# Optimization experiments

Hardware: AMD Instinct MI355X
Metric: run time of the kernel (lower is better)

The kernel has to match this reference:

```python
import jax, jax.numpy as jnp
import numpy as np

N = 50000   # num_nodes
E = 640000  # num_edges (avg degree ~12.8)
D = 128     # input_dim
H = 128     # hidden_dim
T = 100     # targets per head


def setup_inputs() -> dict:
    key = jax.random.key(0)
    ks = jax.random.split(key, 20)
    w = lambda k, s: jax.random.normal(k, s, jnp.float32) * 0.02
    return {
        "x": jax.random.normal(ks[0], (N, D), jnp.float32),
        "edge_index": jax.random.randint(ks[1], (2, E), 0, N, dtype=jnp.int32),
        "edge_weight": jax.random.uniform(ks[2], (E,), jnp.float32),
        "ace_idx": jax.random.randint(ks[3], (T,), 0, N, dtype=jnp.int32),
        "h2_idx": jax.random.randint(ks[4], (T,), 0, N, dtype=jnp.int32),
        "W1": w(ks[5], (D, H)), "b1": jnp.zeros((H,), jnp.float32),
        "W2": w(ks[6], (H, H)), "b2": jnp.zeros((H,), jnp.float32),
        "W3": w(ks[7], (H, H)), "b3": jnp.zeros((H,), jnp.float32),
        "Wh": w(ks[8], (H, H)), "bh": jnp.zeros((H,), jnp.float32),
        "Wace": w(ks[9], (H, 1)), "bace": jnp.zeros((1,), jnp.float32),
        "Wh2": w(ks[10], (H, 1)), "bh2": jnp.zeros((1,), jnp.float32),
    }


def gcn_conv(x, src, dst, ew, W, b):
    # PyG GCNConv: add self-loops (weight 1), symmetric D^-1/2 (A+I) D^-1/2, then XW + b
    n = x.shape[0]
    xw = x @ W                                             # [N, H]
    deg = jax.ops.segment_sum(ew, dst, num_segments=n) + 1.0  # +1 from self-loop
    dinv = jax.lax.rsqrt(jnp.maximum(deg, 1e-12))          # deg >= 1 here
    norm = dinv[src] * ew * dinv[dst]                      # per-edge coefficient
    agg = jax.ops.segment_sum(norm[:, None] * xw[src], dst, num_segments=n)
    agg = agg + (dinv * dinv)[:, None] * xw                # self-loop contribution
    return agg + b


def reference(x, edge_index, edge_weight, ace_idx, h2_idx,
              W1, b1, W2, b2, W3, b3, Wh, bh, Wace, bace, Wh2, bh2):
    src, dst = edge_index[0], edge_index[1]
    h = jax.nn.relu(gcn_conv(x, src, dst, edge_weight, W1, b1))
    h = jax.nn.relu(gcn_conv(h, src, dst, edge_weight, W2, b2))
    h = jax.nn.relu(gcn_conv(h, src, dst, edge_weight, W3, b3))
    # dropout is identity in eval mode
    h = jax.nn.relu(h @ Wh + bh)
    ace_pred = h[ace_idx] @ Wace + bace   # [T, 1]
    h2_pred = h[h2_idx] @ Wh2 + bh2       # [T, 1]
    return jnp.concatenate([ace_pred, h2_pred], axis=0)  # [2T, 1]
```

## Files before the change

### kernel.cpp

```cpp
#include <hip/hip_runtime.h>
#include <math.h>

constexpr int N = 50000;
constexpr int E = 640000;
constexpr int D = 128;
constexpr int T = 100;
constexpr int MAXDEG = 64;
constexpr float SC = 256.0f;
constexpr float SCINV = 1.0f / 256.0f;
constexpr int GB = (N + 127) / 128;
constexpr int EB = (E + 255) / 256;
constexpr int WB = 2 * 16384 / 256;

typedef __attribute__((ext_vector_type(8))) _Float16 half8v;
typedef __attribute__((ext_vector_type(8))) unsigned short ushort8v;
typedef __attribute__((ext_vector_type(4))) float f32x4;

__device__ inline float dinv_of(unsigned int degY) {
  return 1.0f / sqrtf((float)degY * (1.0f / 16777216.0f) + 1.0f);
}


template <bool DINV>
__device__ inline void mfma_core_and_store(
    const unsigned short* __restrict__ Bl, half8v (*a)[2],
    const uint2* __restrict__ degcnt,
    int row0, int rbase, int q, int n16, unsigned short* __restrict__ out) {
  constexpr int SB = 136;
  f32x4 acc[2][8] = {};
#pragma unroll
  for (int kc = 0; kc < 4; ++kc) {
    const int ko = kc * 32 + q * 8;
#pragma unroll
    for (int ct = 0; ct < 8; ++ct) {
      int n = ct * 16 + n16;
      half8v b = *(const half8v*)&Bl[n * SB + ko];
#pragma unroll
      for (int rt = 0; rt < 2; ++rt) {
        acc[rt][ct] = __builtin_amdgcn_mfma_f32_16x16x32_f16(a[kc][rt], b, acc[rt][ct], 0, 0, 0);
      }
    }
  }
#pragma unroll
  for (int rt = 0; rt < 2; ++rt) {
#pragma unroll
    for (int r = 0; r < 4; ++r) {
      int gr = row0 + rbase + rt * 16 + q * 4 + r;
      if (gr < N) {
        float dv = 1.0f;
        if (DINV) dv = dinv_of(degcnt[gr].y);
#pragma unroll
        for (int ct = 0; ct < 8; ++ct) {
          int col = ct * 16 + n16;
          _Float16 h = (_Float16)(DINV ? acc[rt][ct][r] * dv : acc[rt][ct][r]);
          out[(size_t)gr * D + col] = *(unsigned short*)&h;
        }
      }
    }
  }
}


__global__ __launch_bounds__(256) void fused_build_kernel(
    const float* __restrict__ x, const float* __restrict__ W1,
    const float* __restrict__ W2, const float* __restrict__ W3,
    const float* __restrict__ ew, const int* __restrict__ src,
    const int* __restrict__ dst,
    unsigned long long* __restrict__ degcnt, unsigned int* __restrict__ slot,
    unsigned short* __restrict__ wt1, unsigned short* __restrict__ w3kn,
    unsigned short* __restrict__ z1) {
  constexpr int SB = 136;
  __shared__ unsigned short Bl[128 * SB];
  const int b = blockIdx.x;
  const int tid = threadIdx.x;

  if (b < GB) {
#pragma unroll
    for (int it = 0; it < 16; ++it) {
      int idx4 = tid + it * 256;
      int e = idx4 * 4;
      int k = e >> 7, n = e & 127;
      float4 v = *(const float4*)&W1[e];
      _Float16 h0 = (_Float16)(v.x * SC);
      _Float16 h1 = (_Float16)(v.y * SC);
      _Float16 h2 = (_Float16)(v.z * SC);
      _Float16 h3 = (_Float16)(v.w * SC);
      Bl[(n + 0) * SB + k] = *(unsigned short*)&h0;
      Bl[(n + 1) * SB + k] = *(unsigned short*)&h1;
      Bl[(n + 2) * SB + k] = *(unsigned short*)&h2;
      Bl[(n + 3) * SB + k] = *(unsigned short*)&h3;
    }
    __syncthreads();

    const int w = tid >> 6, lane = tid & 63;
    const int q = lane >> 4, n16 = lane & 15;
    const int rbase = w * 32;
    const int row0 = b * 128;
    size_t arow[2];
#pragma unroll
    for (int rt = 0; rt < 2; ++rt) {
      int gr = row0 + rbase + rt * 16 + n16;
      if (gr >= N) gr = N - 1;
      arow[rt] = (size_t)gr * D;
    }
    half8v a[4][2];
#pragma unroll
    for (int kc = 0; kc < 4; ++kc) {
      const int ko = kc * 32 + q * 8;
#pragma unroll
      for (int rt = 0; rt < 2; ++rt) {
        float4 v0 = *(const float4*)&x[arow[rt] + ko];
        float4 v1 = *(const float4*)&x[arow[rt] + ko + 4];
        half8v h;
        h[0] = (_Float16)v0.x; h[1] = (_Float16)v0.y;
        h[2] = (_Float16)v0.z; h[3] = (_Float16)v0.w;
        h[4] = (_Float16)v1.x; h[5] = (_Float16)v1.y;
        h[6] = (_Float16)v1.z; h[7] = (_Float16)v1.w;
        a[kc][rt] = h;
      }
    }
    mfma_core_and_store<false>(Bl, a, nullptr, row0, rbase, q, n16, z1);
  } else if (b < GB + EB) {
    int e = (b - GB) * 256 + tid;
    if (e < E) {
      float w = ew[e];
      int d = dst[e];
      unsigned int fxdeg = __float2uint_rn(w * 16777216.0f);
      unsigned int fx16 = __float2uint_rn(w * 65536.0f);
      if (fx16 > 65535u) fx16 = 65535u;
      unsigned long long old = atomicAdd(&degcnt[d],
                                         ((unsigned long long)fxdeg << 32) | 1ull);
      unsigned int rank = (unsigned int)(old & 0xffffffffull);
      if (rank < MAXDEG)
        slot[(size_t)d * MAXDEG + rank] = (fx16 << 16) | (unsigned int)src[e];
    }
  } else {
    int idx = (b - GB - EB) * 256 + tid;
    int layer = idx >> 14;
    int r = idx & 16383;
    int k = r & 127, n = r >> 7;
    if (layer == 0) {
      _Float16 h = (_Float16)W2[k * D + n];
      wt1[n * D + k] = *(unsigned short*)&h;
    } else {
      _Float16 h = (_Float16)W3[k * D + n];
      w3kn[k * D + n] = *(unsigned short*)&h;
    }
  }
}


__device__ inline void stage_B(const unsigned short* __restrict__ Wt,
                               unsigned short* __restrict__ Bl, int tid) {
  constexpr int SB = 136;
#pragma unroll
  for (int it = 0; it < 8; ++it) {
    int idx = tid + it * 256;
    int r = idx >> 4;
    int c8 = idx & 15;
    ushort8v v = *(const ushort8v*)&Wt[r * D + c8 * 8];
    *(ushort8v*)&Bl[r * SB + c8 * 8] = v;
  }
}

__global__ __launch_bounds__(256) void gemm_mfma_kernel(
    const unsigned short* __restrict__ A, const unsigned short* __restrict__ Wt,
    const uint2* __restrict__ degcnt, unsigned short* __restrict__ out) {
  constexpr int SB = 136;
  __shared__ unsigned short Bl[128 * SB];
  const int tid = threadIdx.x;
  const int row0 = blockIdx.x * 128;
  stage_B(Wt, Bl, tid);
  __syncthreads();

  const int w = tid >> 6, lane = tid & 63;
  const int q = lane >> 4, n16 = lane & 15;
  const int rbase = w * 32;
  size_t arow[2];
#pragma unroll
  for (int rt = 0; rt < 2; ++rt) {
    int gr = row0 + rbase + rt * 16 + n16;
    if (gr >= N) gr = N - 1;
    arow[rt] = (size_t)gr * D;
  }
  half8v a[4][2];
#pragma unroll
  for (int kc = 0; kc < 4; ++kc) {
    const int ko = kc * 32 + q * 8;
#pragma unroll
    for (int rt = 0; rt < 2; ++rt)
      a[kc][rt] = *(const half8v*)&A[arow[rt] + ko];
  }
  mfma_core_and_store<true>(Bl, a, degcnt, row0, rbase, q, n16, out);
}


__global__ __launch_bounds__(256) void agg_kernel(
    const unsigned short* __restrict__ z, const unsigned int* __restrict__ slot,
    const uint2* __restrict__ degcnt, const float* __restrict__ bias,
    unsigned short* __restrict__ oP) {
  int g = (blockIdx.x * 256 + threadIdx.x) >> 4;
  int lane = threadIdx.x & 15;
  const unsigned int* degY = (const unsigned int*)degcnt;

  uint2 pg = degcnt[g];
  int cnt = (int)pg.x; if (cnt > MAXDEG) cnt = MAXDEG;
  float dvg = dinv_of(pg.y);
  half8v xv = *(const half8v*)&z[(size_t)g * D + lane * 8];
  float acc[8];
#pragma unroll
  for (int i = 0; i < 8; ++i) acc[i] = dvg * (float)xv[i];

  const unsigned int* sl = slot + (size_t)g * MAXDEG;
  int k = 0;
  for (; k + 4 <= cnt; k += 4) {
    uint4 p = *(const uint4*)&sl[k];
    float d0 = dinv_of(degY[((p.x & 0xffffu) << 1) + 1]);
    float d1 = dinv_of(degY[((p.y & 0xffffu) << 1) + 1]);
    float d2 = dinv_of(degY[((p.z & 0xffffu) << 1) + 1]);
    float d3 = dinv_of(degY[((p.w & 0xffffu) << 1) + 1]);
    float c0 = (float)(p.x >> 16) * (1.0f / 65536.0f) * d0;
    float c1 = (float)(p.y >> 16) * (1.0f / 65536.0f) * d1;
    float c2 = (float)(p.z >> 16) * (1.0f / 65536.0f) * d2;
    float c3 = (float)(p.w >> 16) * (1.0f / 65536.0f) * d3;
    half8v v0 = *(const half8v*)&z[(size_t)(p.x & 0xffffu) * D + lane * 8];
    half8v v1 = *(const half8v*)&z[(size_t)(p.y & 0xffffu) * D + lane * 8];
    half8v v2 = *(const half8v*)&z[(size_t)(p.z & 0xffffu) * D + lane * 8];
    half8v v3 = *(const half8v*)&z[(size_t)(p.w & 0xffffu) * D + lane * 8];
#pragma unroll
    for (int i = 0; i < 8; ++i) {
      acc[i] = fmaf(c0, (float)v0[i], acc[i]);
      acc[i] = fmaf(c1, (float)v1[i], acc[i]);
      acc[i] = fmaf(c2, (float)v2[i], acc[i]);
      acc[i] = fmaf(c3, (float)v3[i], acc[i]);
    }
  }
  for (; k < cnt; ++k) {
    unsigned int p = sl[k];
    float dsv = dinv_of(degY[((p & 0xffffu) << 1) + 1]);
    float c = (float)(p >> 16) * (1.0f / 65536.0f) * dsv;
    half8v v = *(const half8v*)&z[(size_t)(p & 0xffffu) * D + lane * 8];
#pragma unroll
    for (int i = 0; i < 8; ++i) acc[i] = fmaf(c, (float)v[i], acc[i]);
  }

  half8v hv;
#pragma unroll
  for (int i = 0; i < 8; ++i)
    hv[i] = (_Float16)fmaxf(fmaf(dvg, acc[i], bias[lane * 8 + i] * SC), 0.f);
  *(half8v*)&oP[(size_t)g * D + lane * 8] = hv;
}


__global__ __launch_bounds__(256) void l23_heads_kernel(
    const unsigned short* __restrict__ z2, const unsigned int* __restrict__ slot,
    const uint2* __restrict__ degcnt,
    const float* __restrict__ b2, const float* __restrict__ b3,
    const unsigned short* __restrict__ w3kn,
    const float* __restrict__ Wh, const float* __restrict__ bh,
    const int* __restrict__ ace_idx, const int* __restrict__ h2_idx,
    const float* __restrict__ Wace, const float* __restrict__ bace,
    const float* __restrict__ Wh2, const float* __restrict__ bh2,
    float* __restrict__ out) {
  __shared__ float sacc[16][128];
  __shared__ unsigned short w3l[16384];
  __shared__ float svec[128];
  __shared__ float h3v[128];
  __shared__ float psum[2];
  int t = blockIdx.x;
  int tid = threadIdx.x;
  int node; const float* whead; float bhead;
  if (t < T) { node = ace_idx[t];     whead = Wace; bhead = bace[0]; }
  else       { node = h2_idx[t - T];  whead = Wh2;  bhead = bh2[0]; }

#pragma unroll
  for (int it = 0; it < 8; ++it) {
    int idx = tid + it * 256;
    *(ushort8v*)&w3l[idx * 8] = *(const ushort8v*)&w3kn[idx * 8];
  }

  int grp = tid >> 4, lane = tid & 15;
  float b2l[8];
#pragma unroll
  for (int i = 0; i < 8; ++i) b2l[i] = b2[lane * 8 + i] * SC;

  uint2 pn = degcnt[node];
  int tcnt = (int)pn.x; if (tcnt > MAXDEG) tcnt = MAXDEG;
  float dvn = dinv_of(pn.y);
  const unsigned int* tsl = slot + (size_t)node * MAXDEG;
  int nitems = 1 + tcnt;
  float a[8] = {};
  for (int it = grp; it < nitems; it += 16) {
    int u; float wgt;
    if (it == 0) { u = node; wgt = 1.0f; }
    else {
      unsigned int p = tsl[it - 1];
      wgt = (float)(p >> 16) * (1.0f / 65536.0f);
      u = (int)(p & 0xffffu);
    }
    uint2 pu = degcnt[u];
    float dvu = dinv_of(pu.y);
    int cu = (int)pu.x; if (cu > MAXDEG) cu = MAXDEG;
    half8v xv = *(const half8v*)&z2[(size_t)u * D + lane * 8];
    float r[8];
#pragma unroll
    for (int i = 0; i < 8; ++i) r[i] = (float)xv[i];
    const unsigned int* usl = slot + (size_t)u * MAXDEG;
    int e = 0;
    for (; e + 4 <= cu; e += 4) {
      uint4 p4 = *(const uint4*)&usl[e];
      float c0 = (float)(p4.x >> 16) * (1.0f / 65536.0f);
      float c1 = (float)(p4.y >> 16) * (1.0f / 65536.0f);
      float c2 = (float)(p4.z >> 16) * (1.0f / 65536.0f);
      float c3 = (float)(p4.w >> 16) * (1.0f / 65536.0f);
      half8v v0 = *(const half8v*)&z2[(size_t)(p4.x & 0xffffu) * D + lane * 8];
      half8v v1 = *(const half8v*)&z2[(size_t)(p4.y & 0xffffu) * D + lane * 8];
      half8v v2 = *(const half8v*)&z2[(size_t)(p4.z & 0xffffu) * D + lane * 8];
      half8v v3 = *(const half8v*)&z2[(size_t)(p4.w & 0xffffu) * D + lane * 8];
#pragma unroll
      for (int i = 0; i < 8; ++i) {
        r[i] = fmaf(c0, (float)v0[i], r[i]);
        r[i] = fmaf(c1, (float)v1[i], r[i]);
        r[i] = fmaf(c2, (float)v2[i], r[i]);
        r[i] = fmaf(c3, (float)v3[i], r[i]);
      }
    }
    for (; e < cu; ++e) {
      unsigned int p2 = usl[e];
      float c2 = (float)(p2 >> 16) * (1.0f / 65536.0f);
      half8v v = *(const half8v*)&z2[(size_t)(p2 & 0xffffu) * D + lane * 8];
#pragma unroll
      for (int i = 0; i < 8; ++i) r[i] = fmaf(c2, (float)v[i], r[i]);
    }
#pragma unroll
    for (int i = 0; i < 8; ++i) {
      float h2 = fmaxf(fmaf(dvu, r[i], b2l[i]), 0.f);
      a[i] = fmaf(wgt, dvu * h2, a[i]);
    }
  }
#pragma unroll
  for (int i = 0; i < 8; ++i) sacc[grp][lane * 8 + i] = a[i];
  __syncthreads();

  if (tid < 128) {
    float s = 0.f;
#pragma unroll
    for (int gp = 0; gp < 16; ++gp) s += sacc[gp][tid];
    svec[tid] = s * dvn;
  }
  __syncthreads();

  if (tid < 128) {
    float y = b3[tid] * SC;
#pragma unroll 16
    for (int k = 0; k < 128; ++k) {
      _Float16 wv = *(const _Float16*)&w3l[k * D + tid];
      y = fmaf(svec[k], (float)wv, y);
    }
    h3v[tid] = fmaxf(y, 0.f) * SCINV;
  }
  __syncthreads();

  float v = 0.f;
  if (tid < 128) {
    float acc = bh[tid];
#pragma unroll 16
    for (int k = 0; k < 128; ++k)
      acc = fmaf(h3v[k], Wh[k * D + tid], acc);
    v = fmaxf(acc, 0.f) * whead[tid];
  }
#pragma unroll
  for (int off = 32; off; off >>= 1) v += __shfl_down(v, off, 64);
  if (tid < 128 && (tid & 63) == 0) psum[tid >> 6] = v;
  __syncthreads();
  if (tid == 0) out[t] = psum[0] + psum[1] + bhead;
}


extern "C" void kernel_launch(void* const* d_in, const int* in_sizes, int n_in,
                              void* d_out, int out_size, void* d_ws, size_t ws_size,
                              hipStream_t stream) {
  const float* x    = (const float*)d_in[0];
  const int*   ei   = (const int*)d_in[1];
  const float* ew   = (const float*)d_in[2];
  const int*   ace  = (const int*)d_in[3];
  const int*   h2   = (const int*)d_in[4];
  const float* W1 = (const float*)d_in[5];  const float* b1 = (const float*)d_in[6];
  const float* W2 = (const float*)d_in[7];  const float* b2 = (const float*)d_in[8];
  const float* W3 = (const float*)d_in[9];  const float* b3 = (const float*)d_in[10];
  const float* Wh = (const float*)d_in[11]; const float* bh = (const float*)d_in[12];
  const float* Wace = (const float*)d_in[13]; const float* bace = (const float*)d_in[14];
  const float* Wh2  = (const float*)d_in[15]; const float* bh2  = (const float*)d_in[16];
  const int* src = ei;
  const int* dst = ei + E;

  char* w = (char*)d_ws;
  unsigned long long* degcnt = (unsigned long long*)w;  w += (size_t)N * 8;
  unsigned int* slot = (unsigned int*)w;  w += (size_t)N * MAXDEG * 4;
  unsigned short* wt1 = (unsigned short*)w;  w += 16384 * 2;
  unsigned short* w3kn = (unsigned short*)w; w += 16384 * 2;
  unsigned short* zbuf = (unsigned short*)w; w += (size_t)N * D * 2;
  unsigned short* P1  = (unsigned short*)w;  w += (size_t)N * D * 2;

  const int AG = N * 16 / 256;

  hipMemsetAsync(degcnt, 0, (size_t)N * 8, stream);
  fused_build_kernel<<<GB + EB + WB, 256, 0, stream>>>(
      x, W1, W2, W3, ew, src, dst, degcnt, slot, wt1, w3kn, zbuf);
  agg_kernel<<<AG, 256, 0, stream>>>(zbuf, slot, (const uint2*)degcnt, b1, P1);
  gemm_mfma_kernel<<<GB, 256, 0, stream>>>(P1, wt1, (const uint2*)degcnt, zbuf);
  l23_heads_kernel<<<2 * T, 256, 0, stream>>>(zbuf, slot, (const uint2*)degcnt,
                                              b2, b3, w3kn, Wh, bh, ace, h2,
                                              Wace, bace, Wh2, bh2, (float*)d_out);
}
```

Baseline: 207.1 us.

## Split fused build kernel, replace memset with init kernel, read GEMM B from global

The combined build kernel is split into an init kernel (zeroes degcnt and pre-converts W1/W2/W3 to fp16), a separate edge-pass kernel, and a GEMM kernel that reads the pre-transposed B matrix directly from global/L2 instead of staging it in LDS. This removes the hipMemsetAsync, the per-block W1 transpose, and LDS staging with its barrier, which should also allow higher occupancy. The cost is two extra kernel launches, a serialized edge pass that no longer overlaps the first GEMM, and B fragments fetched from cache by every block.

```diff
diff --git a/kernel.cpp b/kernel.cpp
--- a/kernel.cpp
+++ b/kernel.cpp
@@ -9,8 +9,9 @@
 constexpr float SC = 256.0f;
 constexpr float SCINV = 1.0f / 256.0f;
 constexpr int GB = (N + 127) / 128;
-constexpr int EB = (E + 255) / 256;
-constexpr int WB = 2 * 16384 / 256;
+constexpr int EBLK = (E + 255) / 256;
+constexpr int ZB = N * 8 / 16 / 256 + 1;
+constexpr int WCB = 3 * 16384 / 256;
 
 typedef __attribute__((ext_vector_type(8))) _Float16 half8v;
 typedef __attribute__((ext_vector_type(8))) unsigned short ushort8v;
@@ -21,26 +22,111 @@
 }
 
 
-template <bool DINV>
-__device__ inline void mfma_core_and_store(
-    const unsigned short* __restrict__ Bl, half8v (*a)[2],
-    const uint2* __restrict__ degcnt,
-    int row0, int rbase, int q, int n16, unsigned short* __restrict__ out) {
-  constexpr int SB = 136;
-  f32x4 acc[2][8] = {};
+__global__ __launch_bounds__(256) void init_kernel(
+    const float* __restrict__ W1, const float* __restrict__ W2,
+    const float* __restrict__ W3, uint4* __restrict__ degcnt_v,
+    unsigned short* __restrict__ wt0, unsigned short* __restrict__ wt1,
+    unsigned short* __restrict__ w3kn) {
+  int b = blockIdx.x, tid = threadIdx.x;
+  if (b < ZB) {
+    int i = b * 256 + tid;
+    if (i < N * 8 / 16) degcnt_v[i] = uint4{0, 0, 0, 0};
+  } else {
+    int idx = (b - ZB) * 256 + tid;
+    int layer = idx >> 14;
+    int r = idx & 16383;
+    if (layer == 0) {
+      int n = r >> 7, k = r & 127;
+      _Float16 h = (_Float16)(W1[k * D + n] * SC);
+      wt0[n * D + k] = *(unsigned short*)&h;
+    } else if (layer == 1) {
+      int n = r >> 7, k = r & 127;
+      _Float16 h = (_Float16)W2[k * D + n];
+      wt1[n * D + k] = *(unsigned short*)&h;
+    } else {
+      int k = r >> 7, n = r & 127;
+      _Float16 h = (_Float16)W3[k * D + n];
+      w3kn[k * D + n] = *(unsigned short*)&h;
+    }
+  }
+}
+
+
+__global__ void edge_pass_kernel(const float* __restrict__ ew, const int* __restrict__ src,
+                                 const int* __restrict__ dst,
+                                 unsigned long long* __restrict__ degcnt,
+                                 unsigned int* __restrict__ slot) {
+  int e = blockIdx.x * 256 + threadIdx.x;
+  if (e < E) {
+    float w = ew[e];
+    int d = dst[e];
+    unsigned int fxdeg = __float2uint_rn(w * 16777216.0f);
+    unsigned int fx16 = __float2uint_rn(w * 65536.0f);
+    if (fx16 > 65535u) fx16 = 65535u;
+    unsigned long long old = atomicAdd(&degcnt[d],
+                                       ((unsigned long long)fxdeg << 32) | 1ull);
+    unsigned int rank = (unsigned int)(old & 0xffffffffull);
+    if (rank < MAXDEG)
+      slot[(size_t)d * MAXDEG + rank] = (fx16 << 16) | (unsigned int)src[e];
+  }
+}
+
+
+template <bool F32A, bool DINV>
+__global__ __launch_bounds__(256) void gemm_nolds_kernel(
+    const void* __restrict__ Ain, const unsigned short* __restrict__ Bt,
+    const uint2* __restrict__ degcnt, unsigned short* __restrict__ out) {
+  const int tid = threadIdx.x;
+  const int w = tid >> 6, lane = tid & 63;
+  const int q = lane >> 4, n16 = lane & 15;
+  const int rbase = w * 32;
+  const int row0 = blockIdx.x * 128;
+
+  size_t arow[2];
+#pragma unroll
+  for (int rt = 0; rt < 2; ++rt) {
+    int gr = row0 + rbase + rt * 16 + n16;
+    if (gr >= N) gr = N - 1;
+    arow[rt] = (size_t)gr * D;
+  }
+  half8v a[4][2];
 #pragma unroll
   for (int kc = 0; kc < 4; ++kc) {
     const int ko = kc * 32 + q * 8;
 #pragma unroll
+    for (int rt = 0; rt < 2; ++rt) {
+      if (F32A) {
+        const float* A = (const float*)Ain;
+        float4 v0 = *(const float4*)&A[arow[rt] + ko];
+        float4 v1 = *(const float4*)&A[arow[rt] + ko + 4];
+        half8v h;
+        h[0] = (_Float16)v0.x; h[1] = (_Float16)v0.y;
+        h[2] = (_Float16)v0.z; h[3] = (_Float16)v0.w;
+        h[4] = (_Float16)v1.x; h[5] = (_Float16)v1.y;
+        h[6] = (_Float16)v1.z; h[7] = (_Float16)v1.w;
+        a[kc][rt] = h;
+      } else {
+        const unsigned short* A = (const unsigned short*)Ain;
+        a[kc][rt] = *(const half8v*)&A[arow[rt] + ko];
+      }
+    }
+  }
+
+  f32x4 acc[2][8] = {};
+#pragma unroll
+  for (int kc = 0; kc < 4; ++kc) {
+    const int ko = kc * 32 + q * 8;
+#pragma unroll
     for (int ct = 0; ct < 8; ++ct) {
       int n = ct * 16 + n16;
-      half8v b = *(const half8v*)&Bl[n * SB + ko];
+      half8v b = *(const half8v*)&Bt[n * D + ko];
 #pragma unroll
       for (int rt = 0; rt < 2; ++rt) {
         acc[rt][ct] = __builtin_amdgcn_mfma_f32_16x16x32_f16(a[kc][rt], b, acc[rt][ct], 0, 0, 0);
       }
     }
   }
+
 #pragma unroll
   for (int rt = 0; rt < 2; ++rt) {
 #pragma unroll
@@ -58,140 +144,6 @@
       }
     }
   }
-}
-
-
-__global__ __launch_bounds__(256) void fused_build_kernel(
-    const float* __restrict__ x, const float* __restrict__ W1,
-    const float* __restrict__ W2, const float* __restrict__ W3,
-    const float* __restrict__ ew, const int* __restrict__ src,
-    const int* __restrict__ dst,
-    unsigned long long* __restrict__ degcnt, unsigned int* __restrict__ slot,
-    unsigned short* __restrict__ wt1, unsigned short* __restrict__ w3kn,
-    unsigned short* __restrict__ z1) {
-  constexpr int SB = 136;
-  __shared__ unsigned short Bl[128 * SB];
-  const int b = blockIdx.x;
-  const int tid = threadIdx.x;
-
-  if (b < GB) {
-#pragma unroll
-    for (int it = 0; it < 16; ++it) {
-      int idx4 = tid + it * 256;
-      int e = idx4 * 4;
-      int k = e >> 7, n = e & 127;
-      float4 v = *(const float4*)&W1[e];
-      _Float16 h0 = (_Float16)(v.x * SC);
-      _Float16 h1 = (_Float16)(v.y * SC);
-      _Float16 h2 = (_Float16)(v.z * SC);
-      _Float16 h3 = (_Float16)(v.w * SC);
-      Bl[(n + 0) * SB + k] = *(unsigned short*)&h0;
-      Bl[(n + 1) * SB + k] = *(unsigned short*)&h1;
-      Bl[(n + 2) * SB + k] = *(unsigned short*)&h2;
-      Bl[(n + 3) * SB + k] = *(unsigned short*)&h3;
-    }
-    __syncthreads();
-
-    const int w = tid >> 6, lane = tid & 63;
-    const int q = lane >> 4, n16 = lane & 15;
-    const int rbase = w * 32;
-    const int row0 = b * 128;
-    size_t arow[2];
-#pragma unroll
-    for (int rt = 0; rt < 2; ++rt) {
-      int gr = row0 + rbase + rt * 16 + n16;
-      if (gr >= N) gr = N - 1;
-      arow[rt] = (size_t)gr * D;
-    }
-    half8v a[4][2];
-#pragma unroll
-    for (int kc = 0; kc < 4; ++kc) {
-      const int ko = kc * 32 + q * 8;
-#pragma unroll
-      for (int rt = 0; rt < 2; ++rt) {
-        float4 v0 = *(const float4*)&x[arow[rt] + ko];
-        float4 v1 = *(const float4*)&x[arow[rt] + ko + 4];
-        half8v h;
-        h[0] = (_Float16)v0.x; h[1] = (_Float16)v0.y;
-        h[2] = (_Float16)v0.z; h[3] = (_Float16)v0.w;
-        h[4] = (_Float16)v1.x; h[5] = (_Float16)v1.y;
-        h[6] = (_Float16)v1.z; h[7] = (_Float16)v1.w;
-        a[kc][rt] = h;
-      }
-    }
-    mfma_core_and_store<false>(Bl, a, nullptr, row0, rbase, q, n16, z1);
-  } else if (b < GB + EB) {
-    int e = (b - GB) * 256 + tid;
-    if (e < E) {
-      float w = ew[e];
-      int d = dst[e];
-      unsigned int fxdeg = __float2uint_rn(w * 16777216.0f);
-      unsigned int fx16 = __float2uint_rn(w * 65536.0f);
-      if (fx16 > 65535u) fx16 = 65535u;
-      unsigned long long old = atomicAdd(&degcnt[d],
-                                         ((unsigned long long)fxdeg << 32) | 1ull);
-      unsigned int rank = (unsigned int)(old & 0xffffffffull);
-      if (rank < MAXDEG)
-        slot[(size_t)d * MAXDEG + rank] = (fx16 << 16) | (unsigned int)src[e];
-    }
-  } else {
-    int idx = (b - GB - EB) * 256 + tid;
-    int layer = idx >> 14;
-    int r = idx & 16383;
-    int k = r & 127, n = r >> 7;
-    if (layer == 0) {
-      _Float16 h = (_Float16)W2[k * D + n];
-      wt1[n * D + k] = *(unsigned short*)&h;
-    } else {
-      _Float16 h = (_Float16)W3[k * D + n];
-      w3kn[k * D + n] = *(unsigned short*)&h;
-    }
-  }
-}
-
-
-__device__ inline void stage_B(const unsigned short* __restrict__ Wt,
-                               unsigned short* __restrict__ Bl, int tid) {
-  constexpr int SB = 136;
-#pragma unroll
-  for (int it = 0; it < 8; ++it) {
-    int idx = tid + it * 256;
-    int r = idx >> 4;
-    int c8 = idx & 15;
-    ushort8v v = *(const ushort8v*)&Wt[r * D + c8 * 8];
-    *(ushort8v*)&Bl[r * SB + c8 * 8] = v;
-  }
-}
-
-__global__ __launch_bounds__(256) void gemm_mfma_kernel(
-    const unsigned short* __restrict__ A, const unsigned short* __restrict__ Wt,
-    const uint2* __restrict__ degcnt, unsigned short* __restrict__ out) {
-  constexpr int SB = 136;
-  __shared__ unsigned short Bl[128 * SB];
-  const int tid = threadIdx.x;
-  const int row0 = blockIdx.x * 128;
-  stage_B(Wt, Bl, tid);
-  __syncthreads();
-
-  const int w = tid >> 6, lane = tid & 63;
-  const int q = lane >> 4, n16 = lane & 15;
-  const int rbase = w * 32;
-  size_t arow[2];
-#pragma unroll
-  for (int rt = 0; rt < 2; ++rt) {
-    int gr = row0 + rbase + rt * 16 + n16;
-    if (gr >= N) gr = N - 1;
-    arow[rt] = (size_t)gr * D;
-  }
-  half8v a[4][2];
-#pragma unroll
-  for (int kc = 0; kc < 4; ++kc) {
-    const int ko = kc * 32 + q * 8;
-#pragma unroll
-    for (int rt = 0; rt < 2; ++rt)
-      a[kc][rt] = *(const half8v*)&A[arow[rt] + ko];
-  }
-  mfma_core_and_store<true>(Bl, a, degcnt, row0, rbase, q, n16, out);
 }
 
 
@@ -397,6 +349,7 @@
   char* w = (char*)d_ws;
   unsigned long long* degcnt = (unsigned long long*)w;  w += (size_t)N * 8;
   unsigned int* slot = (unsigned int*)w;  w += (size_t)N * MAXDEG * 4;
+  unsigned short* wt0 = (unsigned short*)w;  w += 16384 * 2;
   unsigned short* wt1 = (unsigned short*)w;  w += 16384 * 2;
   unsigned short* w3kn = (unsigned short*)w; w += 16384 * 2;
   unsigned short* zbuf = (unsigned short*)w; w += (size_t)N * D * 2;
@@ -404,11 +357,11 @@
 
   const int AG = N * 16 / 256;
 
-  hipMemsetAsync(degcnt, 0, (size_t)N * 8, stream);
-  fused_build_kernel<<<GB + EB + WB, 256, 0, stream>>>(
-      x, W1, W2, W3, ew, src, dst, degcnt, slot, wt1, w3kn, zbuf);
+  init_kernel<<<ZB + WCB, 256, 0, stream>>>(W1, W2, W3, (uint4*)degcnt, wt0, wt1, w3kn);
+  edge_pass_kernel<<<EBLK, 256, 0, stream>>>(ew, src, dst, degcnt, slot);
+  gemm_nolds_kernel<true, false><<<GB, 256, 0, stream>>>(x, wt0, nullptr, zbuf);
   agg_kernel<<<AG, 256, 0, stream>>>(zbuf, slot, (const uint2*)degcnt, b1, P1);
-  gemm_mfma_kernel<<<GB, 256, 0, stream>>>(P1, wt1, (const uint2*)degcnt, zbuf);
+  gemm_nolds_kernel<false, true><<<GB, 256, 0, stream>>>(P1, wt1, (const uint2*)degcnt, zbuf);
   l23_heads_kernel<<<2 * T, 256, 0, stream>>>(zbuf, slot, (const uint2*)degcnt,
                                               b2, b3, w3kn, Wh, bh, ace, h2,
                                               Wace, bace, Wh2, bh2, (float*)d_out);
```

New measurement: 216.6 us. 4.6% more time.
